# Optimization experiments

Measured on AMD Instinct MI355X. Metric: run time of the kernel, lower is better.

The kernel has to match this reference:

```python
import jax, jax.numpy as jnp
import numpy as np
from jax import lax

D_MODEL = 768
D_STATE = 16
D_CONV = 4
EXPAND = 1
D_INNER = D_MODEL * EXPAND  # 768
BATCH, SEQ = 8, 4096


def setup_inputs() -> dict:
    key = jax.random.key(0)
    ks = jax.random.split(key, 8)
    s = 0.02
    x = jax.random.normal(ks[0], (BATCH, SEQ, D_MODEL), jnp.float32)
    W_in = jax.random.normal(ks[1], (D_MODEL, 2 * D_INNER), jnp.float32) * s
    conv_w = jax.random.normal(ks[2], (D_INNER, 1, D_CONV), jnp.float32) * s  # depthwise (O, I/groups=1, K)
    W_x = jax.random.normal(ks[3], (D_INNER, D_STATE + D_MODEL), jnp.float32) * s
    A_log = jax.random.normal(ks[4], (D_MODEL, D_STATE), jnp.float32)
    Dp = jnp.ones((D_MODEL,), jnp.float32)
    W_out = jax.random.normal(ks[5], (D_INNER, D_MODEL), jnp.float32) * s
    gamma = jnp.ones((D_MODEL,), jnp.float32)
    beta = jnp.zeros((D_MODEL,), jnp.float32)
    return {"x": x, "W_in": W_in, "conv_w": conv_w, "W_x": W_x,
            "A_log": A_log, "Dp": Dp, "W_out": W_out, "gamma": gamma, "beta": beta}


def _layernorm(x, gamma, beta, eps=1e-5):
    mu = x.mean(-1, keepdims=True)
    var = ((x - mu) ** 2).mean(-1, keepdims=True)
    return (x - mu) * lax.rsqrt(var + eps) * gamma + beta


def reference(x, W_in, conv_w, W_x, A_log, Dp, W_out, gamma, beta):
    residual = x
    xn = _layernorm(x, gamma, beta)
    xz = xn @ W_in                                  # (b, l, 2*d_inner)
    x1, z = jnp.split(xz, 2, axis=-1)               # each (b, l, d_inner)
    # depthwise causal conv1d (left pad d_conv-1, truncate to L == causal)
    xc = jnp.transpose(x1, (0, 2, 1))               # (b, c, l)
    xc = lax.conv_general_dilated(
        xc, conv_w, window_strides=(1,), padding=[(D_CONV - 1, 0)],
        dimension_numbers=("NCH", "OIH", "NCH"), feature_group_count=D_INNER)
    x1 = jnp.transpose(xc, (0, 2, 1))               # (b, l, d_inner)
    ssm = x1 @ W_x                                  # (b, l, d_state + d_model)
    Bm = ssm[..., :D_STATE]                         # (b, l, d_state)
    Cm = ssm[..., D_STATE:]                         # (b, l, d_model)
    A = -jnp.exp(A_log)                             # (d_model, d_state)
    # pseudo-SSM mixing (valid-einsum interpretation of the source)
    h = jnp.einsum('bln,nd->bld', x1, A) + Bm * x1.sum(-1, keepdims=True)  # (b, l, d_state)
    y = Cm * h.sum(-1, keepdims=True) + Dp * x1     # (b, l, d_inner)
    y = y * jax.nn.silu(z)
    return y @ W_out + residual
```

## Files before the change

### kernel.cpp

```cpp
#include <hip/hip_runtime.h>

typedef __bf16 bf16_t;
typedef __bf16 bf16x8 __attribute__((ext_vector_type(8)));
typedef __bf16 bf16x4 __attribute__((ext_vector_type(4)));
typedef float f32x4 __attribute__((ext_vector_type(4)));

#define DM 768
#define SEQ_LEN 4096
#define TOKENS 32768

__device__ __forceinline__ void load16_to_lds(const void* g, void* l) {
  __builtin_amdgcn_global_load_lds(
      (const __attribute__((address_space(1))) unsigned int*)g,
      (__attribute__((address_space(3))) unsigned int*)l, 16, 0, 0);
}

__global__ __launch_bounds__(256)
void cast_transpose_kernel(const float* __restrict__ W, bf16_t* __restrict__ WT,
                           int K, int N, int stride, int off) {
  long idx = (long)blockIdx.x * 256 + threadIdx.x;
  if (idx >= (long)K * N) return;
  int n = (int)(idx / K);
  int k = (int)(idx % K);
  WT[idx] = (bf16_t)W[(long)k * stride + off + n];
}

__global__ __launch_bounds__(256)
void ab_kernel(const float* __restrict__ Wx, const float* __restrict__ A_log,
               float* __restrict__ a_vec, float* __restrict__ b_vec) {
  int k = blockIdx.x * 256 + threadIdx.x;
  if (k >= DM) return;
  float a = 0.f, b = 0.f;
#pragma unroll
  for (int d = 0; d < 16; d++) {
    a -= __expf(A_log[k * 16 + d]);
    b += Wx[(long)k * 784 + d];
  }
  a_vec[k] = a;
  b_vec[k] = b;
}

__global__ __launch_bounds__(256)
void ln_kernel(const float* __restrict__ x, const float* __restrict__ gamma,
               const float* __restrict__ beta, bf16_t* __restrict__ xn) {
  const int tok = blockIdx.x * 4 + (threadIdx.x >> 6);
  const int lane = threadIdx.x & 63;
  const float4* xr = (const float4*)(x + (long)tok * DM);
  float4 v0 = xr[lane], v1 = xr[lane + 64], v2 = xr[lane + 128];
  float s = v0.x + v0.y + v0.z + v0.w + v1.x + v1.y + v1.z + v1.w +
            v2.x + v2.y + v2.z + v2.w;
  float ss = v0.x * v0.x + v0.y * v0.y + v0.z * v0.z + v0.w * v0.w +
             v1.x * v1.x + v1.y * v1.y + v1.z * v1.z + v1.w * v1.w +
             v2.x * v2.x + v2.y * v2.y + v2.z * v2.z + v2.w * v2.w;
  for (int o = 1; o < 64; o <<= 1) { s += __shfl_xor(s, o); ss += __shfl_xor(ss, o); }
  float mu = s * (1.0f / DM);
  float var = ss * (1.0f / DM) - mu * mu;
  float inv = rsqrtf(var + 1e-5f);
  const float4* g4 = (const float4*)gamma;
  const float4* b4 = (const float4*)beta;
  bf16_t* xo = xn + (long)tok * DM;
#pragma unroll
  for (int i = 0; i < 3; i++) {
    float4 v = (i == 0) ? v0 : (i == 1) ? v1 : v2;
    float4 g = g4[lane + 64 * i], b = b4[lane + 64 * i];
    bf16x4 o;
    o[0] = (bf16_t)((v.x - mu) * inv * g.x + b.x);
    o[1] = (bf16_t)((v.y - mu) * inv * g.y + b.y);
    o[2] = (bf16_t)((v.z - mu) * inv * g.z + b.z);
    o[3] = (bf16_t)((v.w - mu) * inv * g.w + b.w);
    *(bf16x4*)(xo + lane * 4 + i * 256) = o;
  }
}

__global__ __launch_bounds__(256)
void conv_kernel(const bf16_t* __restrict__ xz, const float* __restrict__ conv_w,
                 const float* __restrict__ a_vec, const float* __restrict__ b_vec,
                 bf16_t* __restrict__ x1, float* __restrict__ hs) {
  const int tok = blockIdx.x * 4 + (threadIdx.x >> 6);
  const int lane = threadIdx.x & 63;
  const int l = tok & (SEQ_LEN - 1);
  const bf16_t* base = xz + (long)tok * 1536;
  const float4* w4 = (const float4*)conv_w;
  float s = 0.f, sa = 0.f, sb = 0.f;

  {
    const int c0 = lane * 8;
    bf16x8 cur = *(const bf16x8*)(base + c0);
    bf16x8 p1 = {}, p2 = {}, p3 = {};
    if (l >= 1) p1 = *(const bf16x8*)(base + c0 - 1536);
    if (l >= 2) p2 = *(const bf16x8*)(base + c0 - 2 * 1536);
    if (l >= 3) p3 = *(const bf16x8*)(base + c0 - 3 * 1536);
    bf16x8 o;
#pragma unroll
    for (int j = 0; j < 8; j++) {
      float4 w = w4[c0 + j];
      float acc = w.w * (float)cur[j] + w.z * (float)p1[j] +
                  w.y * (float)p2[j] + w.x * (float)p3[j];
      bf16_t xb = (bf16_t)acc;
      o[j] = xb;
      float xv = (float)xb;
      s += xv; sa += xv * a_vec[c0 + j]; sb += xv * b_vec[c0 + j];
    }
    *(bf16x8*)(x1 + (long)tok * DM + c0) = o;
  }
  {
    const int c0 = 512 + lane * 4;
    bf16x4 cur = *(const bf16x4*)(base + c0);
    bf16x4 p1 = {}, p2 = {}, p3 = {};
    if (l >= 1) p1 = *(const bf16x4*)(base + c0 - 1536);
    if (l >= 2) p2 = *(const bf16x4*)(base + c0 - 2 * 1536);
    if (l >= 3) p3 = *(const bf16x4*)(base + c0 - 3 * 1536);
    bf16x4 o;
#pragma unroll
    for (int j = 0; j < 4; j++) {
      float4 w = w4[c0 + j];
      float acc = w.w * (float)cur[j] + w.z * (float)p1[j] +
                  w.y * (float)p2[j] + w.x * (float)p3[j];
      bf16_t xb = (bf16_t)acc;
      o[j] = xb;
      float xv = (float)xb;
      s += xv; sa += xv * a_vec[c0 + j]; sb += xv * b_vec[c0 + j];
    }
    *(bf16x4*)(x1 + (long)tok * DM + c0) = o;
  }
  for (int o = 1; o < 64; o <<= 1) {
    s += __shfl_xor(s, o); sa += __shfl_xor(sa, o); sb += __shfl_xor(sb, o);
  }
  if (lane == 0) hs[tok] = sa + s * sb;
}

template <int OUT_MODE>
__global__ __launch_bounds__(256, 3)
void gemm128_kernel(const bf16_t* __restrict__ A, const bf16_t* __restrict__ BT,
                    void* __restrict__ outp, const float* __restrict__ res,
                    const bf16_t* __restrict__ x1, const bf16_t* __restrict__ xz,
                    const float* __restrict__ hs, const float* __restrict__ Dp,
                    int M, int N, int K) {
  __shared__ __align__(16) bf16_t As[128 * 32];
  __shared__ __align__(16) bf16_t Bs[128 * 32];

  const int nby = N >> 7;
  const int nwg = (M >> 7) * nby;
  const int cpx = nwg >> 3;
  const int wg = blockIdx.x;
  const int swz = (wg & 7) * cpx + (wg >> 3);
  const int bx = swz / nby;
  const int by = swz - bx * nby;
  const int m0 = bx << 7;
  const int n0 = by << 7;

  const int t = threadIdx.x;
  const int lane = t & 63;
  const int wave = t >> 6;
  const int wm = (wave >> 1) * 64;
  const int wn = (wave & 1) * 64;
  const int l15 = lane & 15;
  const int quad = lane >> 4;

  f32x4 acc[4][4] = {};

  const int sr = lane >> 2;
  const int sc = (lane & 3) * 8;
  const bf16_t* Ag[2];
  bf16_t* lA[2];
#pragma unroll
  for (int i = 0; i < 2; i++) {
    int ch = wave * 2 + i;
    Ag[i] = A + (long)(m0 + ch * 16 + sr) * K + sc;
    lA[i] = As + ch * 512 + lane * 8;
  }
  const bf16_t* Bg[2];
  bf16_t* lB[2];
#pragma unroll
  for (int i = 0; i < 2; i++) {
    int ch = wave * 2 + i;
    Bg[i] = BT + (long)(n0 + ch * 16 + sr) * K + sc;
    lB[i] = Bs + ch * 512 + lane * 8;
  }

  for (int k0 = 0; k0 < K; k0 += 32) {
#pragma unroll
    for (int i = 0; i < 2; i++) load16_to_lds(Ag[i] + k0, lA[i]);
#pragma unroll
    for (int i = 0; i < 2; i++) load16_to_lds(Bg[i] + k0, lB[i]);
    __syncthreads();
    bf16x8 bfrag[4];
#pragma unroll
    for (int ni = 0; ni < 4; ni++)
      bfrag[ni] = *(const bf16x8*)&Bs[(wn + ni * 16 + l15) * 32 + quad * 8];
#pragma unroll
    for (int mi = 0; mi < 4; mi++) {
      bf16x8 afrag = *(const bf16x8*)&As[(wm + mi * 16 + l15) * 32 + quad * 8];
#pragma unroll
      for (int ni = 0; ni < 4; ni++)
        acc[mi][ni] = __builtin_amdgcn_mfma_f32_16x16x32_bf16(afrag, bfrag[ni], acc[mi][ni], 0, 0, 0);
    }
    __syncthreads();
  }

#pragma unroll
  for (int mi = 0; mi < 4; mi++) {
#pragma unroll
    for (int r = 0; r < 4; r++) {
      const int row = m0 + wm + mi * 16 + quad * 4 + r;
      float hsv = 0.f;
      if (OUT_MODE == 1) hsv = hs[row];
#pragma unroll
      for (int ni = 0; ni < 4; ni++) {
        const int col = n0 + wn + ni * 16 + l15;
        const long o = (long)row * N + col;
        float v = acc[mi][ni][r];
        if (OUT_MODE == 0) {
          ((bf16_t*)outp)[o] = (bf16_t)v;
        } else if (OUT_MODE == 1) {
          float xv = (float)x1[(long)row * DM + col];
          float zv = (float)xz[(long)row * 1536 + DM + col];
          float yv = v * hsv + Dp[col] * xv;
          yv *= zv / (1.f + __expf(-zv));
          ((bf16_t*)outp)[o] = (bf16_t)yv;
        } else {
          ((float*)outp)[o] = v + res[o];
        }
      }
    }
  }
}

extern "C" void kernel_launch(void* const* d_in, const int* in_sizes, int n_in,
                              void* d_out, int out_size, void* d_ws, size_t ws_size,
                              hipStream_t stream) {
  const float* x      = (const float*)d_in[0];
  const float* W_in   = (const float*)d_in[1];
  const float* conv_w = (const float*)d_in[2];
  const float* W_x    = (const float*)d_in[3];
  const float* A_log  = (const float*)d_in[4];
  const float* Dp     = (const float*)d_in[5];
  const float* W_out  = (const float*)d_in[6];
  const float* gamma  = (const float*)d_in[7];
  const float* beta   = (const float*)d_in[8];
  float* out = (float*)d_out;

  char* ws = (char*)d_ws;
  bf16_t* w_in_T  = (bf16_t*)(ws + 0);
  bf16_t* w_c_T   = (bf16_t*)(ws + 2359296);
  bf16_t* w_out_T = (bf16_t*)(ws + 3538944);
  float*  a_vec   = (float*)(ws + 4718592);
  float*  b_vec   = (float*)(ws + 4721664);
  float*  hs      = (float*)(ws + 4724736);
  bf16_t* xn      = (bf16_t*)(ws + 4855808);
  bf16_t* xz      = (bf16_t*)(ws + 55187456);
  bf16_t* x1      = (bf16_t*)(ws + 155850752);
  bf16_t* y       = xn;

  cast_transpose_kernel<<<dim3(1536 * 768 / 256), 256, 0, stream>>>(W_in, w_in_T, 768, 1536, 1536, 0);
  cast_transpose_kernel<<<dim3(768 * 768 / 256), 256, 0, stream>>>(W_x, w_c_T, 768, 768, 784, 16);
  cast_transpose_kernel<<<dim3(768 * 768 / 256), 256, 0, stream>>>(W_out, w_out_T, 768, 768, 768, 0);
  ab_kernel<<<dim3(3), 256, 0, stream>>>(W_x, A_log, a_vec, b_vec);

  ln_kernel<<<dim3(TOKENS / 4), 256, 0, stream>>>(x, gamma, beta, xn);

  gemm128_kernel<0><<<dim3((TOKENS / 128) * (1536 / 128)), 256, 0, stream>>>(
      xn, w_in_T, (void*)xz, nullptr, nullptr, nullptr, nullptr, nullptr,
      TOKENS, 1536, 768);

  conv_kernel<<<dim3(TOKENS / 4), 256, 0, stream>>>(xz, conv_w, a_vec, b_vec, x1, hs);

  gemm128_kernel<1><<<dim3((TOKENS / 128) * (768 / 128)), 256, 0, stream>>>(
      x1, w_c_T, (void*)y, nullptr, x1, xz, hs, Dp,
      TOKENS, 768, 768);

  gemm128_kernel<2><<<dim3((TOKENS / 128) * (768 / 128)), 256, 0, stream>>>(
      y, w_out_T, (void*)out, x, nullptr, nullptr, nullptr, nullptr,
      TOKENS, 768, 768);
}
```

Measured before the change: 496.5 us.

## Double-buffer LDS tiles in GEMM to overlap global loads with MFMA

Splits the A and B shared-memory tiles into two ping-pong buffers and prefetches the next K-tile with direct-to-LDS loads while MFMAs run on the current one. Partial vmcnt waits plus raw s_barrier replace the full __syncthreads, so the next tile's loads can stay in flight during compute. This doubles LDS use per block, which may reduce occupancy under launch_bounds(256,3). It also depends on the vmcnt bookkeeping matching the compiler's instruction order.

```diff
diff --git a/kernel.cpp b/kernel.cpp
--- a/kernel.cpp
+++ b/kernel.cpp
@@ -136,8 +136,8 @@
                     const bf16_t* __restrict__ x1, const bf16_t* __restrict__ xz,
                     const float* __restrict__ hs, const float* __restrict__ Dp,
                     int M, int N, int K) {
-  __shared__ __align__(16) bf16_t As[128 * 32];
-  __shared__ __align__(16) bf16_t Bs[128 * 32];
+  __shared__ __align__(16) bf16_t As[2][128 * 32];
+  __shared__ __align__(16) bf16_t Bs[2][128 * 32];
 
   const int nby = N >> 7;
   const int nwg = (M >> 7) * nby;
@@ -162,40 +162,64 @@
   const int sr = lane >> 2;
   const int sc = (lane & 3) * 8;
   const bf16_t* Ag[2];
-  bf16_t* lA[2];
+  const bf16_t* Bg[2];
+  int lOff[2];
 #pragma unroll
   for (int i = 0; i < 2; i++) {
     int ch = wave * 2 + i;
     Ag[i] = A + (long)(m0 + ch * 16 + sr) * K + sc;
-    lA[i] = As + ch * 512 + lane * 8;
-  }
-  const bf16_t* Bg[2];
-  bf16_t* lB[2];
-#pragma unroll
-  for (int i = 0; i < 2; i++) {
-    int ch = wave * 2 + i;
     Bg[i] = BT + (long)(n0 + ch * 16 + sr) * K + sc;
-    lB[i] = Bs + ch * 512 + lane * 8;
-  }
-
-  for (int k0 = 0; k0 < K; k0 += 32) {
-#pragma unroll
-    for (int i = 0; i < 2; i++) load16_to_lds(Ag[i] + k0, lA[i]);
-#pragma unroll
-    for (int i = 0; i < 2; i++) load16_to_lds(Bg[i] + k0, lB[i]);
-    __syncthreads();
+    lOff[i] = ch * 512 + lane * 8;
+  }
+
+  const int NT = K >> 5;
+
+#pragma unroll
+  for (int i = 0; i < 2; i++) load16_to_lds(Ag[i], &As[0][lOff[i]]);
+#pragma unroll
+  for (int i = 0; i < 2; i++) load16_to_lds(Bg[i], &Bs[0][lOff[i]]);
+
+  for (int kt = 0; kt < NT - 1; kt++) {
+    const int cur = kt & 1;
+    const int nxt = cur ^ 1;
+    const int k1 = (kt + 1) << 5;
+#pragma unroll
+    for (int i = 0; i < 2; i++) load16_to_lds(Ag[i] + k1, &As[nxt][lOff[i]]);
+#pragma unroll
+    for (int i = 0; i < 2; i++) load16_to_lds(Bg[i] + k1, &Bs[nxt][lOff[i]]);
+    asm volatile("s_waitcnt vmcnt(4)" ::: "memory");
+    __builtin_amdgcn_s_barrier();
+    asm volatile("" ::: "memory");
     bf16x8 bfrag[4];
 #pragma unroll
     for (int ni = 0; ni < 4; ni++)
-      bfrag[ni] = *(const bf16x8*)&Bs[(wn + ni * 16 + l15) * 32 + quad * 8];
+      bfrag[ni] = *(const bf16x8*)&Bs[cur][(wn + ni * 16 + l15) * 32 + quad * 8];
 #pragma unroll
     for (int mi = 0; mi < 4; mi++) {
-      bf16x8 afrag = *(const bf16x8*)&As[(wm + mi * 16 + l15) * 32 + quad * 8];
+      bf16x8 afrag = *(const bf16x8*)&As[cur][(wm + mi * 16 + l15) * 32 + quad * 8];
 #pragma unroll
       for (int ni = 0; ni < 4; ni++)
         acc[mi][ni] = __builtin_amdgcn_mfma_f32_16x16x32_bf16(afrag, bfrag[ni], acc[mi][ni], 0, 0, 0);
     }
-    __syncthreads();
+    asm volatile("" ::: "memory");
+    __builtin_amdgcn_s_barrier();
+  }
+  {
+    const int cur = (NT - 1) & 1;
+    asm volatile("s_waitcnt vmcnt(0)" ::: "memory");
+    __builtin_amdgcn_s_barrier();
+    asm volatile("" ::: "memory");
+    bf16x8 bfrag[4];
+#pragma unroll
+    for (int ni = 0; ni < 4; ni++)
+      bfrag[ni] = *(const bf16x8*)&Bs[cur][(wn + ni * 16 + l15) * 32 + quad * 8];
+#pragma unroll
+    for (int mi = 0; mi < 4; mi++) {
+      bf16x8 afrag = *(const bf16x8*)&As[cur][(wm + mi * 16 + l15) * 32 + quad * 8];
+#pragma unroll
+      for (int ni = 0; ni < 4; ni++)
+        acc[mi][ni] = __builtin_amdgcn_mfma_f32_16x16x32_bf16(afrag, bfrag[ni], acc[mi][ni], 0, 0, 0);
+    }
   }
 
 #pragma unroll
```

Result: no change. 498.2 us (+0.3%).

## Replace 128x128 GEMM with double-buffered 256x256 tile, 8-wave pipelined MFMA kernel

Applied to the files above, without the earlier changes.

Replaces the simple 128x128, single-buffered GEMM with a 256x256 tile kernel using 512 threads, a K-step of 64 and a two-buffer LDS ring. It uses XOR-swizzled LDS layout to avoid bank conflicts and interleaves global-to-LDS staging with MFMA quadrants, using s_setprio around the MFMA blocks. The aim is to raise arithmetic intensity and hide load latency behind compute in all three GEMMs. The costs are far more LDS (128KB per block) and more registers, which lowers occupancy, and the grid shrinks to fewer, larger workgroups.

```diff
diff --git a/kernel.cpp b/kernel.cpp
--- a/kernel.cpp
+++ b/kernel.cpp
@@ -130,76 +130,152 @@
 }
 
 template <int OUT_MODE>
-__global__ __launch_bounds__(256, 3)
-void gemm128_kernel(const bf16_t* __restrict__ A, const bf16_t* __restrict__ BT,
+__global__ __launch_bounds__(512, 2)
+void gemm256_kernel(const bf16_t* __restrict__ A, const bf16_t* __restrict__ BT,
                     void* __restrict__ outp, const float* __restrict__ res,
                     const bf16_t* __restrict__ x1, const bf16_t* __restrict__ xz,
                     const float* __restrict__ hs, const float* __restrict__ Dp,
                     int M, int N, int K) {
-  __shared__ __align__(16) bf16_t As[128 * 32];
-  __shared__ __align__(16) bf16_t Bs[128 * 32];
-
-  const int nby = N >> 7;
-  const int nwg = (M >> 7) * nby;
+  __shared__ __align__(16) bf16_t As[2][256 * 64];
+  __shared__ __align__(16) bf16_t Bs[2][256 * 64];
+
+  const int nby = N >> 8;
+  const int nwg = (M >> 8) * nby;
   const int cpx = nwg >> 3;
   const int wg = blockIdx.x;
   const int swz = (wg & 7) * cpx + (wg >> 3);
   const int bx = swz / nby;
   const int by = swz - bx * nby;
-  const int m0 = bx << 7;
-  const int n0 = by << 7;
+  const int m0 = bx << 8;
+  const int n0 = by << 8;
 
   const int t = threadIdx.x;
   const int lane = t & 63;
   const int wave = t >> 6;
-  const int wm = (wave >> 1) * 64;
-  const int wn = (wave & 1) * 64;
+  const int wm = (wave >> 2) * 128;
+  const int wn = (wave & 3) * 64;
   const int l15 = lane & 15;
   const int quad = lane >> 4;
 
-  f32x4 acc[4][4] = {};
-
-  const int sr = lane >> 2;
-  const int sc = (lane & 3) * 8;
-  const bf16_t* Ag[2];
-  bf16_t* lA[2];
-#pragma unroll
-  for (int i = 0; i < 2; i++) {
-    int ch = wave * 2 + i;
-    Ag[i] = A + (long)(m0 + ch * 16 + sr) * K + sc;
-    lA[i] = As + ch * 512 + lane * 8;
-  }
-  const bf16_t* Bg[2];
-  bf16_t* lB[2];
-#pragma unroll
-  for (int i = 0; i < 2; i++) {
-    int ch = wave * 2 + i;
-    Bg[i] = BT + (long)(n0 + ch * 16 + sr) * K + sc;
-    lB[i] = Bs + ch * 512 + lane * 8;
-  }
-
-  for (int k0 = 0; k0 < K; k0 += 32) {
-#pragma unroll
-    for (int i = 0; i < 2; i++) load16_to_lds(Ag[i] + k0, lA[i]);
-#pragma unroll
-    for (int i = 0; i < 2; i++) load16_to_lds(Bg[i] + k0, lB[i]);
-    __syncthreads();
-    bf16x8 bfrag[4];
-#pragma unroll
-    for (int ni = 0; ni < 4; ni++)
-      bfrag[ni] = *(const bf16x8*)&Bs[(wn + ni * 16 + l15) * 32 + quad * 8];
-#pragma unroll
-    for (int mi = 0; mi < 4; mi++) {
-      bf16x8 afrag = *(const bf16x8*)&As[(wm + mi * 16 + l15) * 32 + quad * 8];
-#pragma unroll
-      for (int ni = 0; ni < 4; ni++)
-        acc[mi][ni] = __builtin_amdgcn_mfma_f32_16x16x32_bf16(afrag, bfrag[ni], acc[mi][ni], 0, 0, 0);
-    }
-    __syncthreads();
-  }
-
-#pragma unroll
-  for (int mi = 0; mi < 4; mi++) {
+  const int sx0 = (((0 * 4) + quad) ^ (lane & 7)) * 8;
+  const int sx1 = (((1 * 4) + quad) ^ (lane & 7)) * 8;
+
+  const int srow = lane >> 3;
+  const int scol = (((lane & 7) ^ ((lane >> 3) & 7))) * 8;
+
+  f32x4 acc[8][4] = {};
+  bf16x8 a[4][2], b0[2][2], b1[2][2];
+
+  const bf16_t* Abase = A + (long)m0 * K + scol;
+  const bf16_t* Bbase = BT + (long)n0 * K + scol;
+
+#define STAGE_A(buf, kt) do {                                               \
+    const long kk_ = (long)(kt) * 64;                                       \
+    _Pragma("unroll")                                                       \
+    for (int h_ = 0; h_ < 2; h_++) {                                        \
+      _Pragma("unroll")                                                     \
+      for (int j_ = 0; j_ < 2; j_++) {                                      \
+        const int rowl_ = h_ * 128 + wave * 16 + j_ * 8;                    \
+        load16_to_lds(Abase + (long)(rowl_ + srow) * K + kk_,               \
+                      &As[buf][rowl_ * 64]);                                \
+      } } } while (0)
+
+#define STAGE_B(buf, kt) do {                                               \
+    const long kk_ = (long)(kt) * 64;                                       \
+    _Pragma("unroll")                                                       \
+    for (int h_ = 0; h_ < 2; h_++) {                                        \
+      _Pragma("unroll")                                                     \
+      for (int j_ = 0; j_ < 2; j_++) {                                      \
+        const int rowl_ = h_ * 128 + wave * 16 + j_ * 8;                    \
+        load16_to_lds(Bbase + (long)(rowl_ + srow) * K + kk_,               \
+                      &Bs[buf][rowl_ * 64]);                                \
+      } } } while (0)
+
+#define READ_A(qm, buf) do {                                                \
+    _Pragma("unroll")                                                       \
+    for (int mi_ = 0; mi_ < 4; mi_++) {                                     \
+      const bf16_t* p_ = &As[buf][(wm + (qm) * 64 + mi_ * 16 + l15) * 64];  \
+      a[mi_][0] = *(const bf16x8*)(p_ + sx0);                               \
+      a[mi_][1] = *(const bf16x8*)(p_ + sx1);                               \
+    } } while (0)
+
+#define READ_B(dst, qn, buf) do {                                           \
+    _Pragma("unroll")                                                       \
+    for (int ni_ = 0; ni_ < 2; ni_++) {                                     \
+      const bf16_t* p_ = &Bs[buf][(wn + (qn) * 32 + ni_ * 16 + l15) * 64];  \
+      dst[ni_][0] = *(const bf16x8*)(p_ + sx0);                             \
+      dst[ni_][1] = *(const bf16x8*)(p_ + sx1);                             \
+    } } while (0)
+
+#define MFMA16(qm, qn, breg) do {                                           \
+    __builtin_amdgcn_s_setprio(1);                                          \
+    _Pragma("unroll")                                                       \
+    for (int mi_ = 0; mi_ < 4; mi_++) {                                     \
+      _Pragma("unroll")                                                     \
+      for (int ni_ = 0; ni_ < 2; ni_++) {                                   \
+        acc[(qm) * 4 + mi_][(qn) * 2 + ni_] =                               \
+            __builtin_amdgcn_mfma_f32_16x16x32_bf16(                        \
+                a[mi_][0], breg[ni_][0],                                    \
+                acc[(qm) * 4 + mi_][(qn) * 2 + ni_], 0, 0, 0);              \
+        acc[(qm) * 4 + mi_][(qn) * 2 + ni_] =                               \
+            __builtin_amdgcn_mfma_f32_16x16x32_bf16(                        \
+                a[mi_][1], breg[ni_][1],                                    \
+                acc[(qm) * 4 + mi_][(qn) * 2 + ni_], 0, 0, 0);              \
+      } }                                                                   \
+    __builtin_amdgcn_s_setprio(0);                                          \
+  } while (0)
+
+#define BAR() do { asm volatile("" ::: "memory");                           \
+    __builtin_amdgcn_s_barrier();                                           \
+    asm volatile("" ::: "memory"); } while (0)
+
+#define VM0() asm volatile("s_waitcnt vmcnt(0)" ::: "memory")
+
+  const int NT = K >> 6;
+  const int NI = NT >> 1;
+
+  STAGE_A(0, 0);
+  STAGE_B(0, 0);
+  VM0();
+  BAR();
+
+  for (int it = 0; it < NI; ++it) {
+    const int t1k = 2 * it + 1;
+    const int t2k = 2 * it + 2;
+    STAGE_A(1, t1k);
+    READ_A(0, 0);
+    READ_B(b0, 0, 0);
+    MFMA16(0, 0, b0);
+    BAR();
+    STAGE_B(1, t1k);
+    READ_B(b1, 1, 0);
+    MFMA16(0, 1, b1);
+    BAR();
+    READ_A(1, 0);
+    MFMA16(1, 1, b1);
+    BAR();
+    MFMA16(1, 0, b0);
+    VM0();
+    BAR();
+    if (t2k < NT) STAGE_A(0, t2k);
+    READ_A(0, 1);
+    READ_B(b0, 0, 1);
+    MFMA16(0, 0, b0);
+    BAR();
+    if (t2k < NT) STAGE_B(0, t2k);
+    READ_B(b1, 1, 1);
+    MFMA16(0, 1, b1);
+    BAR();
+    READ_A(1, 1);
+    MFMA16(1, 1, b1);
+    BAR();
+    MFMA16(1, 0, b0);
+    VM0();
+    BAR();
+  }
+
+#pragma unroll
+  for (int mi = 0; mi < 8; mi++) {
 #pragma unroll
     for (int r = 0; r < 4; r++) {
       const int row = m0 + wm + mi * 16 + quad * 4 + r;
@@ -224,6 +300,13 @@
       }
     }
   }
+#undef STAGE_A
+#undef STAGE_B
+#undef READ_A
+#undef READ_B
+#undef MFMA16
+#undef BAR
+#undef VM0
 }
 
 extern "C" void kernel_launch(void* const* d_in, const int* in_sizes, int n_in,
@@ -259,17 +342,17 @@
 
   ln_kernel<<<dim3(TOKENS / 4), 256, 0, stream>>>(x, gamma, beta, xn);
 
-  gemm128_kernel<0><<<dim3((TOKENS / 128) * (1536 / 128)), 256, 0, stream>>>(
+  gemm256_kernel<0><<<dim3((TOKENS / 256) * (1536 / 256)), 512, 0, stream>>>(
       xn, w_in_T, (void*)xz, nullptr, nullptr, nullptr, nullptr, nullptr,
       TOKENS, 1536, 768);
 
   conv_kernel<<<dim3(TOKENS / 4), 256, 0, stream>>>(xz, conv_w, a_vec, b_vec, x1, hs);
 
-  gemm128_kernel<1><<<dim3((TOKENS / 128) * (768 / 128)), 256, 0, stream>>>(
+  gemm256_kernel<1><<<dim3((TOKENS / 256) * (768 / 256)), 512, 0, stream>>>(
       x1, w_c_T, (void*)y, nullptr, x1, xz, hs, Dp,
       TOKENS, 768, 768);
 
-  gemm128_kernel<2><<<dim3((TOKENS / 128) * (768 / 128)), 256, 0, stream>>>(
+  gemm256_kernel<2><<<dim3((TOKENS / 256) * (768 / 256)), 512, 0, stream>>>(
       y, w_out_T, (void*)out, x, nullptr, nullptr, nullptr, nullptr,
       TOKENS, 768, 768);
 }
```

Result: slower. 530.4 us (+6.8%).
